# Performance work log

Hardware: AMD Instinct MI355X
Metric: run time of the kernel (lower is better)

## Reference

```python
import jax, jax.numpy as jnp
import numpy as np

B, S, E = 512, 200, 128
NUM_C = 1024
DIFF = 100


def _glorot(k, shape):
    fan_in, fan_out = shape[-1], shape[0]
    lim = jnp.sqrt(6.0 / (fan_in + fan_out)).astype(jnp.float32)
    return jax.random.uniform(k, shape, jnp.float32, -lim, lim)


def setup_inputs() -> dict:
    key = jax.random.key(0)
    ks = jax.random.split(key, 16)
    c = jax.random.randint(ks[0], (B, S), 0, NUM_C + 1)
    sd = jax.random.randint(ks[1], (B, S), 0, DIFF + 2)
    a = jax.random.randint(ks[2], (B, S), 0, 2)
    cshft = jax.random.randint(ks[3], (B, S), 0, NUM_C + 1)
    sdshft = jax.random.randint(ks[4], (B, S), 0, DIFF + 2)
    # embedding tables (padding_idx=0 rows zeroed, as in nn.Embedding)
    c_table = _glorot(ks[5], (NUM_C + 1, E)).at[0].set(0.0)
    sd_table = _glorot(ks[6], (DIFF + 2, E)).at[0].set(0.0)
    a_table = _glorot(ks[7], (2, E))
    knowledge = _glorot(ks[8], (1, E))  # xavier_uniform [1, E]
    W1 = _glorot(ks[9], (E, 2 * E)); b1 = jnp.zeros((E,), jnp.float32)
    W2 = _glorot(ks[10], (E, E));     b2 = jnp.zeros((E,), jnp.float32)
    W3 = _glorot(ks[11], (E, E));     b3 = jnp.zeros((E,), jnp.float32)
    W4 = _glorot(ks[12], (E, 2 * E)); b4 = jnp.zeros((E,), jnp.float32)
    W5 = _glorot(ks[13], (E, 2 * E)); b5 = jnp.zeros((E,), jnp.float32)
    W6 = _glorot(ks[14], (E, 3 * E)); b6 = jnp.zeros((E,), jnp.float32)
    return dict(c=c, sd=sd, a=a, cshft=cshft, sdshft=sdshft,
                c_table=c_table, sd_table=sd_table, a_table=a_table,
                knowledge=knowledge,
                W1=W1, b1=b1, W2=W2, b2=b2, W3=W3, b3=b3,
                W4=W4, b4=b4, W5=W5, b5=b5, W6=W6, b6=b6)


def reference(c, sd, a, cshft, sdshft, c_table, sd_table, a_table, knowledge,
              W1, b1, W2, b2, W3, b3, W4, b4, W5, b5, W6, b6):
    # embedding lookups: [B, S, E]
    c_emb = c_table[c]
    sd_emb = sd_table[sd]
    a_emb = a_table[a]
    target_c = c_table[cshft]
    target_sd = sd_table[sdshft]

    input_data = jnp.concatenate((c_emb, sd_emb), -1) @ W1.T + b1      # [B,S,E]
    target_data = jnp.concatenate((target_c, target_sd), -1) @ W1.T + b1

    k0 = jnp.broadcast_to(knowledge, (c.shape[0], knowledge.shape[-1]))  # [B,E]

    def step(k, xs):
        sd_t, a_t, in_t = xs                       # each [B,E]
        qq = k - in_t
        gates_SDF = jax.nn.sigmoid(qq @ W2.T + b2)
        SDFt = gates_SDF * jnp.tanh(qq @ W3.T + b3)  # dropout = eval-mode identity
        x = jnp.concatenate((SDFt, a_t), -1)
        gates_PKA = jax.nn.sigmoid(x @ W4.T + b4)
        PKAt = gates_PKA * jnp.tanh(x @ W5.T + b5)
        ins = jnp.concatenate((k, a_t, sd_t), -1)
        gates_KSU = jax.nn.sigmoid(ins @ W6.T + b6)
        k_new = gates_KSU * k + (1.0 - gates_KSU) * PKAt
        return k_new, k_new

    xs = (jnp.swapaxes(sd_emb, 0, 1),      # [S,B,E]
          jnp.swapaxes(a_emb, 0, 1),
          jnp.swapaxes(input_data, 0, 1))
    _, hs = jax.lax.scan(step, k0, xs)     # hs: [S,B,E]
    output = jnp.swapaxes(hs, 0, 1)        # [B,S,E]

    logits = jnp.sum(target_data * output, axis=-1)  # [B,S]
    return jax.nn.sigmoid(logits)
```

## Files before the change

### kernel.cpp

```cpp
#include <hip/hip_runtime.h>


#define S_ 200
#define E_ 128
#define RS 136

typedef float  float4v __attribute__((ext_vector_type(4)));
typedef _Float16 f16x8 __attribute__((ext_vector_type(8)));

__device__ __forceinline__ float fast_sigmoid(float x) {
  return __builtin_amdgcn_rcpf(1.f + __expf(-x));
}
__device__ __forceinline__ float fast_tanh(float x) {
  return 2.f * __builtin_amdgcn_rcpf(1.f + __expf(-2.f * x)) - 1.f;
}

#define DPP_ADD(x, ctrl) \
  ((x) + __builtin_bit_cast(float, __builtin_amdgcn_update_dpp( \
       0, __builtin_bit_cast(int, (x)), (ctrl), 0xf, 0xf, true)))

__device__ __forceinline__ f16x8 cvt8(const float* __restrict__ p) {
  float4v a = *(const float4v*)p;
  float4v b = *(const float4v*)(p + 4);
  f16x8 r;
  r[0] = (_Float16)a[0]; r[1] = (_Float16)a[1];
  r[2] = (_Float16)a[2]; r[3] = (_Float16)a[3];
  r[4] = (_Float16)b[0]; r[5] = (_Float16)b[1];
  r[6] = (_Float16)b[2]; r[7] = (_Float16)b[3];
  return r;
}

__global__ __launch_bounds__(256) void dimkt_prep(
    const float* __restrict__ c_table, const float* __restrict__ sd_table,
    const float* __restrict__ a_table,
    const float* __restrict__ W1, const float* __restrict__ b1,
    const float* __restrict__ W4, const float* __restrict__ b4,
    const float* __restrict__ W5, const float* __restrict__ b5,
    const float* __restrict__ W6, const float* __restrict__ b6,
    float* __restrict__ ws) {
  __shared__ __attribute__((aligned(16))) float s_src[8][E_];
  __shared__ float s_w[E_][33];
  const int blk = blockIdx.x, t = threadIdx.x;
  const int e = t & 127, h = t >> 7;
  const float* src; const float* wb; const float* bias; float* dst;
  int r0, maxrow, wstr, woff;
  if (blk < 129)      { r0 = blk * 8;       src = c_table;  maxrow = 1024; wb = W1; wstr = 256; woff = 0;   bias = nullptr; dst = ws; }
  else if (blk < 142) { r0 = (blk-129) * 8; src = sd_table; maxrow = 101;  wb = W1; wstr = 256; woff = 128; bias = b1;      dst = ws + 131200; }
  else if (blk < 155) { r0 = (blk-142) * 8; src = sd_table; maxrow = 101;  wb = W6; wstr = 384; woff = 256; bias = nullptr; dst = ws + 144256; }
  else if (blk == 155){ r0 = 0;             src = a_table;  maxrow = 1;    wb = W4; wstr = 256; woff = 128; bias = b4;      dst = ws + 157312; }
  else if (blk == 156){ r0 = 0;             src = a_table;  maxrow = 1;    wb = W5; wstr = 256; woff = 128; bias = b5;      dst = ws + 157568; }
  else                { r0 = 0;             src = a_table;  maxrow = 1;    wb = W6; wstr = 384; woff = 128; bias = b6;      dst = ws + 157824; }
  #pragma unroll
  for (int i = 0; i < 4; ++i) {
    int idx = i * 256 + t, row = idx >> 7, col = idx & 127;
    int rr = r0 + row; if (rr > maxrow) rr = maxrow;
    s_src[row][col] = src[rr * E_ + col];
  }
  float binit = bias ? bias[e] : 0.f;
  float acc[4] = {binit, binit, binit, binit};
  for (int k0 = 0; k0 < 4; ++k0) {
    __syncthreads();
    #pragma unroll
    for (int i = 0; i < 16; ++i) {
      int idx = i * 256 + t;
      s_w[idx >> 5][idx & 31] = wb[(idx >> 5) * wstr + woff + k0 * 32 + (idx & 31)];
    }
    __syncthreads();
    #pragma unroll 4
    for (int kk = 0; kk < 32; ++kk) {
      float wv = s_w[e][kk];
      #pragma unroll
      for (int g = 0; g < 4; ++g)
        acc[g] += wv * s_src[h * 4 + g][k0 * 32 + kk];
    }
  }
  #pragma unroll
  for (int g = 0; g < 4; ++g) {
    int row = r0 + h * 4 + g;
    if (row <= maxrow) dst[row * E_ + e] = acc[g];
  }
}

__global__ __launch_bounds__(512, 2) void dimkt_scan(
    const int* __restrict__ c, const int* __restrict__ sd, const int* __restrict__ a,
    const int* __restrict__ cshft, const int* __restrict__ sdshft,
    const float* __restrict__ knowledge,
    const float* __restrict__ W2, const float* __restrict__ b2,
    const float* __restrict__ W3, const float* __restrict__ b3,
    const float* __restrict__ W4, const float* __restrict__ W5,
    const float* __restrict__ W6,
    const float* __restrict__ ws, float* __restrict__ out) {

  const float* __restrict__ C1  = ws;
  const float* __restrict__ SD1 = ws + 131200;
  const float* __restrict__ SD6 = ws + 144256;
  const float* __restrict__ A4  = ws + 157312;
  const float* __restrict__ A5  = ws + 157568;
  const float* __restrict__ A6  = ws + 157824;

  const int tid  = threadIdx.x;
  const int w    = tid >> 6;
  const int lane = tid & 63;
  const int l15  = lane & 15;
  const int q    = lane >> 4;
  const int qodd = q & 1;
  const int e    = w * 16 + l15;
  const int j    = q >> 1;
  const int bj   = blockIdx.x * 2 + j;

  __shared__ __attribute__((aligned(16))) _Float16 A1[16 * RS];
  __shared__ __attribute__((aligned(16))) _Float16 A2[16 * RS];
  __shared__ __attribute__((aligned(16))) int idx_lds[S_][2][8];
  __shared__ float olog[S_][2];
  __shared__ float red[8][2];

  for (int i = tid; i < 16 * RS; i += 512) { A1[i] = (_Float16)0.f; A2[i] = (_Float16)0.f; }

  for (int i = tid; i < 2 * S_; i += 512) {
    const int jj = (i >= S_) ? 1 : 0;
    const int ss = jj ? (i - S_) : i;
    const int src = (blockIdx.x * 2 + jj) * S_ + ss;
    idx_lds[ss][jj][0] = c[src];
    idx_lds[ss][jj][1] = sd[src];
    idx_lds[ss][jj][2] = a[src];
    idx_lds[ss][jj][3] = cshft[src];
    idx_lds[ss][jj][4] = sdshft[src];
  }

  const int stq = (j * 8) * RS + e;
  const int stk = stq + RS;
  const int rd0 = l15 * RS + q * 8;
  const bool m1 = (l15 & 6) == 0;
  const bool m2 = (l15 & 7) == 0;

  f16x8 w2f[4], w3f[4], w4f[4], w5f[4], w6f[4];
  #pragma unroll
  for (int t = 0; t < 4; ++t) {
    const int ko = t * 32 + q * 8;
    w2f[t] = cvt8(W2 + e * 128 + ko);
    w3f[t] = cvt8(W3 + e * 128 + ko);
    w4f[t] = cvt8(W4 + e * 256 + ko);
    w5f[t] = cvt8(W5 + e * 256 + ko);
    w6f[t] = cvt8(W6 + e * 384 + ko);
  }
  const float b2e = b2[e], b3e = b3[e];
  const float A4t0 = A4[e], A4t1 = A4[E_ + e];
  const float A5t0 = A5[e], A5t1 = A5[E_ + e];
  const float A6t0 = A6[e], A6t1 = A6[E_ + e];

  float kreg = knowledge[e];

  const int base = bj * S_;
  int ic = c[base], isd = sd[base], ia = a[base], ict = cshft[base], ist = sdshft[base];
  float inT  = C1[ic * E_ + e] + SD1[isd * E_ + e];
  float sd6v = SD6[isd * E_ + e];
  float a4v = ia ? A4t1 : A4t0;
  float a5v = ia ? A5t1 : A5t0;
  float a6v = ia ? A6t1 : A6t0;
  float tgt  = C1[ict * E_ + e] + SD1[ist * E_ + e];
  int nic = c[base + 1], nisd = sd[base + 1], nia = a[base + 1],
      nict = cshft[base + 1], nist = sdshft[base + 1];

  __syncthreads();
  if (!qodd) {
    A1[stq] = (_Float16)(kreg - inT);
    A1[stk] = (_Float16)kreg;
  }
  __syncthreads();

  f16x8 f0{}, f1{}, f2{}, f3{};
  f16x8 g0{}, g1{}, g2v{}, g3{};

  float4v acc2{0.f,0.f,0.f,0.f}, acc3{0.f,0.f,0.f,0.f}, acc6{0.f,0.f,0.f,0.f};
  float4v acc4{0.f,0.f,0.f,0.f}, acc5{0.f,0.f,0.f,0.f};

  #pragma unroll 1
  for (int s = 0; s < S_; ++s) {
    if (m1) {
      f0 = *(const f16x8*)&A1[rd0];
      f1 = *(const f16x8*)&A1[rd0 + 32];
      f2 = *(const f16x8*)&A1[rd0 + 64];
      f3 = *(const f16x8*)&A1[rd0 + 96];
    }

    float ninT = C1[nic * E_ + e] + SD1[nisd * E_ + e];
    float nsd6 = SD6[nisd * E_ + e];
    float na4 = nia ? A4t1 : A4t0;
    float na5 = nia ? A5t1 : A5t0;
    float na6 = nia ? A6t1 : A6t0;
    float ntg  = C1[nict * E_ + e] + SD1[nist * E_ + e];

    const int s2 = (s + 2 < S_) ? (s + 2) : (S_ - 1);
    const int4 iv = *(const int4*)&idx_lds[s2][j][0];
    const int tist = idx_lds[s2][j][4];

    acc2[0] = b2e;
    acc3[0] = b3e;
    acc6[1] = a6v + sd6v;
    acc2 = __builtin_amdgcn_mfma_f32_16x16x32_f16(f0, w2f[0], acc2, 0, 0, 0);
    acc3 = __builtin_amdgcn_mfma_f32_16x16x32_f16(f0, w3f[0], acc3, 0, 0, 0);
    acc6 = __builtin_amdgcn_mfma_f32_16x16x32_f16(f0, w6f[0], acc6, 0, 0, 0);
    acc2 = __builtin_amdgcn_mfma_f32_16x16x32_f16(f1, w2f[1], acc2, 0, 0, 0);
    acc3 = __builtin_amdgcn_mfma_f32_16x16x32_f16(f1, w3f[1], acc3, 0, 0, 0);
    acc6 = __builtin_amdgcn_mfma_f32_16x16x32_f16(f1, w6f[1], acc6, 0, 0, 0);
    acc2 = __builtin_amdgcn_mfma_f32_16x16x32_f16(f2, w2f[2], acc2, 0, 0, 0);
    acc3 = __builtin_amdgcn_mfma_f32_16x16x32_f16(f2, w3f[2], acc3, 0, 0, 0);
    acc6 = __builtin_amdgcn_mfma_f32_16x16x32_f16(f2, w6f[2], acc6, 0, 0, 0);
    acc2 = __builtin_amdgcn_mfma_f32_16x16x32_f16(f3, w2f[3], acc2, 0, 0, 0);
    acc3 = __builtin_amdgcn_mfma_f32_16x16x32_f16(f3, w3f[3], acc3, 0, 0, 0);
    acc6 = __builtin_amdgcn_mfma_f32_16x16x32_f16(f3, w6f[3], acc6, 0, 0, 0);

    const float g2  = fast_sigmoid(acc2[0]);
    const float th3 = fast_tanh(acc3[0]);
    const float g6  = fast_sigmoid(acc6[1]);
    const float sdfv = g2 * th3;
    if (!qodd) A2[stq] = (_Float16)sdfv;
    __syncthreads();

    if (m2) {
      g0  = *(const f16x8*)&A2[rd0];
      g1  = *(const f16x8*)&A2[rd0 + 32];
      g2v = *(const f16x8*)&A2[rd0 + 64];
      g3  = *(const f16x8*)&A2[rd0 + 96];
    }

    acc4[0] = a4v;
    acc5[0] = a5v;
    acc4 = __builtin_amdgcn_mfma_f32_16x16x32_f16(g0, w4f[0], acc4, 0, 0, 0);
    acc5 = __builtin_amdgcn_mfma_f32_16x16x32_f16(g0, w5f[0], acc5, 0, 0, 0);
    acc4 = __builtin_amdgcn_mfma_f32_16x16x32_f16(g1, w4f[1], acc4, 0, 0, 0);
    acc5 = __builtin_amdgcn_mfma_f32_16x16x32_f16(g1, w5f[1], acc5, 0, 0, 0);
    acc4 = __builtin_amdgcn_mfma_f32_16x16x32_f16(g2v, w4f[2], acc4, 0, 0, 0);
    acc5 = __builtin_amdgcn_mfma_f32_16x16x32_f16(g2v, w5f[2], acc5, 0, 0, 0);
    acc4 = __builtin_amdgcn_mfma_f32_16x16x32_f16(g3, w4f[3], acc4, 0, 0, 0);
    acc5 = __builtin_amdgcn_mfma_f32_16x16x32_f16(g3, w5f[3], acc5, 0, 0, 0);

    const float pka  = fast_sigmoid(acc4[0]) * fast_tanh(acc5[0]);
    const float knew = pka + g6 * (kreg - pka);
    kreg = knew;
    if (!qodd) {
      A1[stq] = (_Float16)(knew - ninT);
      A1[stk] = (_Float16)knew;
    }

    float p = tgt * knew;
    p = DPP_ADD(p, 0x111);
    p = DPP_ADD(p, 0x112);
    p = DPP_ADD(p, 0x114);
    p = DPP_ADD(p, 0x118);
    if (l15 == 15 && !qodd) red[w][j] = p;

    inT = ninT; sd6v = nsd6; a4v = na4; a5v = na5; a6v = na6; tgt = ntg;
    nic = iv.x; nisd = iv.y; nia = iv.z; nict = iv.w; nist = tist;

    __syncthreads();

    if (tid == 0 || tid == 32) {
      const int jj = tid >> 5;
      float logit = 0.f;
      #pragma unroll
      for (int x = 0; x < 8; ++x) logit += red[x][jj];
      olog[s][jj] = fast_sigmoid(logit);
    }
  }

  __syncthreads();
  for (int i = tid; i < 2 * S_; i += 512) {
    const int jj = (i >= S_) ? 1 : 0;
    const int ss = jj ? (i - S_) : i;
    out[(blockIdx.x * 2 + jj) * S_ + ss] = olog[ss][jj];
  }
}

extern "C" void kernel_launch(void* const* d_in, const int* in_sizes, int n_in,
                              void* d_out, int out_size, void* d_ws, size_t ws_size,
                              hipStream_t stream) {
  const int*   c         = (const int*)  d_in[0];
  const int*   sd        = (const int*)  d_in[1];
  const int*   a         = (const int*)  d_in[2];
  const int*   cshft     = (const int*)  d_in[3];
  const int*   sdshft    = (const int*)  d_in[4];
  const float* c_table   = (const float*)d_in[5];
  const float* sd_table  = (const float*)d_in[6];
  const float* a_table   = (const float*)d_in[7];
  const float* knowledge = (const float*)d_in[8];
  const float* W1 = (const float*)d_in[9];  const float* b1 = (const float*)d_in[10];
  const float* W2 = (const float*)d_in[11]; const float* b2 = (const float*)d_in[12];
  const float* W3 = (const float*)d_in[13]; const float* b3 = (const float*)d_in[14];
  const float* W4 = (const float*)d_in[15]; const float* b4 = (const float*)d_in[16];
  const float* W5 = (const float*)d_in[17]; const float* b5 = (const float*)d_in[18];
  const float* W6 = (const float*)d_in[19]; const float* b6 = (const float*)d_in[20];
  float* ws  = (float*)d_ws;
  float* out = (float*)d_out;
  (void)in_sizes; (void)n_in; (void)out_size; (void)ws_size;

  dimkt_prep<<<158, 256, 0, stream>>>(c_table, sd_table, a_table,
                                      W1, b1, W4, b4, W5, b5, W6, b6, ws);
  dimkt_scan<<<256, 512, 0, stream>>>(c, sd, a, cshft, sdshft, knowledge,
                                      W2, b2, W3, b3, W4, W5, W6, ws, out);
}
```

Measured before the change: 267.6 us.

## Defer logit reduction out of recurrence loop and interleave MFMA chains with activations

The per-step logit dot-product reduction now runs one iteration late, off the critical path. Per-wave partials are stored in an [8][2][S] shared array and summed with the sigmoid once after the loop, which removes the per-step serial tail done by two threads. The MFMA chains are reordered so the W6 gate and the acc4/acc5 activations overlap with other matrix ops. __syncthreads is replaced by an inline s_waitcnt+s_barrier macro. The zero-init of the A1/A2 shared buffers is also removed, which relies on the masked lanes' padding values not mattering.

```diff
diff --git a/kernel.cpp b/kernel.cpp
--- a/kernel.cpp
+++ b/kernel.cpp
@@ -7,6 +7,8 @@
 
 typedef float  float4v __attribute__((ext_vector_type(4)));
 typedef _Float16 f16x8 __attribute__((ext_vector_type(8)));
+
+#define BAR() asm volatile("s_waitcnt lgkmcnt(0)\n\ts_barrier" ::: "memory")
 
 __device__ __forceinline__ float fast_sigmoid(float x) {
   return __builtin_amdgcn_rcpf(1.f + __expf(-x));
@@ -110,11 +112,8 @@
 
   __shared__ __attribute__((aligned(16))) _Float16 A1[16 * RS];
   __shared__ __attribute__((aligned(16))) _Float16 A2[16 * RS];
-  __shared__ __attribute__((aligned(16))) int idx_lds[S_][2][8];
-  __shared__ float olog[S_][2];
-  __shared__ float red[8][2];
-
-  for (int i = tid; i < 16 * RS; i += 512) { A1[i] = (_Float16)0.f; A2[i] = (_Float16)0.f; }
+  __shared__ __attribute__((aligned(32))) int idx_lds[S_][2][8];
+  __shared__ float part[8][2][S_];
 
   for (int i = tid; i < 2 * S_; i += 512) {
     const int jj = (i >= S_) ? 1 : 0;
@@ -174,6 +173,9 @@
   float4v acc2{0.f,0.f,0.f,0.f}, acc3{0.f,0.f,0.f,0.f}, acc6{0.f,0.f,0.f,0.f};
   float4v acc4{0.f,0.f,0.f,0.f}, acc5{0.f,0.f,0.f,0.f};
 
+  float pprev = 0.f;
+  int   sprev = 0;
+
   #pragma unroll 1
   for (int s = 0; s < S_; ++s) {
     if (m1) {
@@ -183,6 +185,15 @@
       f3 = *(const f16x8*)&A1[rd0 + 96];
     }
 
+    if (s > 0) {
+      float pr = pprev;
+      pr = DPP_ADD(pr, 0x111);
+      pr = DPP_ADD(pr, 0x112);
+      pr = DPP_ADD(pr, 0x114);
+      pr = DPP_ADD(pr, 0x118);
+      if (l15 == 15 && !qodd) part[w][j][sprev] = pr;
+    }
+
     float ninT = C1[nic * E_ + e] + SD1[nisd * E_ + e];
     float nsd6 = SD6[nisd * E_ + e];
     float na4 = nia ? A4t1 : A4t0;
@@ -196,26 +207,28 @@
 
     acc2[0] = b2e;
     acc3[0] = b3e;
-    acc6[1] = a6v + sd6v;
     acc2 = __builtin_amdgcn_mfma_f32_16x16x32_f16(f0, w2f[0], acc2, 0, 0, 0);
     acc3 = __builtin_amdgcn_mfma_f32_16x16x32_f16(f0, w3f[0], acc3, 0, 0, 0);
-    acc6 = __builtin_amdgcn_mfma_f32_16x16x32_f16(f0, w6f[0], acc6, 0, 0, 0);
     acc2 = __builtin_amdgcn_mfma_f32_16x16x32_f16(f1, w2f[1], acc2, 0, 0, 0);
     acc3 = __builtin_amdgcn_mfma_f32_16x16x32_f16(f1, w3f[1], acc3, 0, 0, 0);
-    acc6 = __builtin_amdgcn_mfma_f32_16x16x32_f16(f1, w6f[1], acc6, 0, 0, 0);
     acc2 = __builtin_amdgcn_mfma_f32_16x16x32_f16(f2, w2f[2], acc2, 0, 0, 0);
     acc3 = __builtin_amdgcn_mfma_f32_16x16x32_f16(f2, w3f[2], acc3, 0, 0, 0);
-    acc6 = __builtin_amdgcn_mfma_f32_16x16x32_f16(f2, w6f[2], acc6, 0, 0, 0);
     acc2 = __builtin_amdgcn_mfma_f32_16x16x32_f16(f3, w2f[3], acc2, 0, 0, 0);
     acc3 = __builtin_amdgcn_mfma_f32_16x16x32_f16(f3, w3f[3], acc3, 0, 0, 0);
-    acc6 = __builtin_amdgcn_mfma_f32_16x16x32_f16(f3, w6f[3], acc6, 0, 0, 0);
+
+    acc6[1] = a6v + sd6v;
+    acc6 = __builtin_amdgcn_mfma_f32_16x16x32_f16(f0, w6f[0], acc6, 0, 0, 0);
+    acc6 = __builtin_amdgcn_mfma_f32_16x16x32_f16(f1, w6f[1], acc6, 0, 0, 0);
 
     const float g2  = fast_sigmoid(acc2[0]);
     const float th3 = fast_tanh(acc3[0]);
-    const float g6  = fast_sigmoid(acc6[1]);
     const float sdfv = g2 * th3;
     if (!qodd) A2[stq] = (_Float16)sdfv;
-    __syncthreads();
+
+    acc6 = __builtin_amdgcn_mfma_f32_16x16x32_f16(f2, w6f[2], acc6, 0, 0, 0);
+    acc6 = __builtin_amdgcn_mfma_f32_16x16x32_f16(f3, w6f[3], acc6, 0, 0, 0);
+
+    BAR();
 
     if (m2) {
       g0  = *(const f16x8*)&A2[rd0];
@@ -224,18 +237,24 @@
       g3  = *(const f16x8*)&A2[rd0 + 96];
     }
 
+    const float g6 = fast_sigmoid(acc6[1]);
+
     acc4[0] = a4v;
+    acc4 = __builtin_amdgcn_mfma_f32_16x16x32_f16(g0, w4f[0], acc4, 0, 0, 0);
+    acc4 = __builtin_amdgcn_mfma_f32_16x16x32_f16(g1, w4f[1], acc4, 0, 0, 0);
+    acc4 = __builtin_amdgcn_mfma_f32_16x16x32_f16(g2v, w4f[2], acc4, 0, 0, 0);
+    acc4 = __builtin_amdgcn_mfma_f32_16x16x32_f16(g3, w4f[3], acc4, 0, 0, 0);
     acc5[0] = a5v;
-    acc4 = __builtin_amdgcn_mfma_f32_16x16x32_f16(g0, w4f[0], acc4, 0, 0, 0);
     acc5 = __builtin_amdgcn_mfma_f32_16x16x32_f16(g0, w5f[0], acc5, 0, 0, 0);
-    acc4 = __builtin_amdgcn_mfma_f32_16x16x32_f16(g1, w4f[1], acc4, 0, 0, 0);
     acc5 = __builtin_amdgcn_mfma_f32_16x16x32_f16(g1, w5f[1], acc5, 0, 0, 0);
-    acc4 = __builtin_amdgcn_mfma_f32_16x16x32_f16(g2v, w4f[2], acc4, 0, 0, 0);
+
+    const float s4 = fast_sigmoid(acc4[0]);
+
     acc5 = __builtin_amdgcn_mfma_f32_16x16x32_f16(g2v, w5f[2], acc5, 0, 0, 0);
-    acc4 = __builtin_amdgcn_mfma_f32_16x16x32_f16(g3, w4f[3], acc4, 0, 0, 0);
     acc5 = __builtin_amdgcn_mfma_f32_16x16x32_f16(g3, w5f[3], acc5, 0, 0, 0);
 
-    const float pka  = fast_sigmoid(acc4[0]) * fast_tanh(acc5[0]);
+    const float t5  = fast_tanh(acc5[0]);
+    const float pka = s4 * t5;
     const float knew = pka + g6 * (kreg - pka);
     kreg = knew;
     if (!qodd) {
@@ -243,32 +262,32 @@
       A1[stk] = (_Float16)knew;
     }
 
-    float p = tgt * knew;
-    p = DPP_ADD(p, 0x111);
-    p = DPP_ADD(p, 0x112);
-    p = DPP_ADD(p, 0x114);
-    p = DPP_ADD(p, 0x118);
-    if (l15 == 15 && !qodd) red[w][j] = p;
+    pprev = tgt * knew;
+    sprev = s;
 
     inT = ninT; sd6v = nsd6; a4v = na4; a5v = na5; a6v = na6; tgt = ntg;
     nic = iv.x; nisd = iv.y; nia = iv.z; nict = iv.w; nist = tist;
 
-    __syncthreads();
-
-    if (tid == 0 || tid == 32) {
-      const int jj = tid >> 5;
-      float logit = 0.f;
-      #pragma unroll
-      for (int x = 0; x < 8; ++x) logit += red[x][jj];
-      olog[s][jj] = fast_sigmoid(logit);
-    }
+    BAR();
+  }
+
+  {
+    float pr = pprev;
+    pr = DPP_ADD(pr, 0x111);
+    pr = DPP_ADD(pr, 0x112);
+    pr = DPP_ADD(pr, 0x114);
+    pr = DPP_ADD(pr, 0x118);
+    if (l15 == 15 && !qodd) part[w][j][sprev] = pr;
   }
 
   __syncthreads();
   for (int i = tid; i < 2 * S_; i += 512) {
     const int jj = (i >= S_) ? 1 : 0;
     const int ss = jj ? (i - S_) : i;
-    out[(blockIdx.x * 2 + jj) * S_ + ss] = olog[ss][jj];
+    float logit = 0.f;
+    #pragma unroll
+    for (int x = 0; x < 8; ++x) logit += part[x][jj][ss];
+    out[(blockIdx.x * 2 + jj) * S_ + ss] = fast_sigmoid(logit);
   }
 }
 
```

New measurement: 262.1 us, median of 2. 2.0% less time.
